# Kernel optimization log

Hardware: AMD Instinct MI355X
Metric: run time of the kernel (lower is better)

The kernel has to match this reference:

```python
import jax, jax.numpy as jnp
import numpy as np


def rotary_pos_emb(x):
    # x: [b, h, l, k]; interleaved rotary embedding (pairs are (0,1),(2,3),...)
    dim = x.shape[-1]
    seq = x.shape[-2]
    ts = jnp.arange(0, dim, 2, dtype=jnp.float32)
    inv_freqs = 10000.0 ** (-ts / dim)                      # [dim/2]
    grid = jnp.arange(seq, dtype=jnp.float32)[:, None] * inv_freqs[None, :]  # [l, dim/2]
    sin_embs = jnp.repeat(jnp.sin(grid), 2, axis=-1)[None]  # [1, l, dim] (interleaved repeat)
    cos_embs = jnp.repeat(jnp.cos(grid), 2, axis=-1)[None]
    x1, x2 = x[..., ::2], x[..., 1::2]
    xs = jnp.stack([-x2, x1], axis=-1).reshape(x.shape)     # interleave (-x2, x1)
    return x * cos_embs + xs * sin_embs


def setup_inputs() -> dict:
    key = jax.random.key(0)
    ks = jax.random.split(key, 5)
    b, l, d = 2, 2048, 1024
    scale = 1.0 / np.sqrt(d)
    return {
        "x": jax.random.normal(ks[0], (b, l, d), dtype=jnp.float32),
        "Wq": jax.random.normal(ks[1], (d, d), dtype=jnp.float32) * scale,
        "Wk": jax.random.normal(ks[2], (d, d), dtype=jnp.float32) * scale,
        "Wv": jax.random.normal(ks[3], (d, d), dtype=jnp.float32) * scale,
        "Wo": jax.random.normal(ks[4], (d, d), dtype=jnp.float32) * scale,
        "is_training": 0,
    }


def reference(x, Wq, Wk, Wv, Wo, is_training):
    n_heads = 16
    b, l, d = x.shape
    k_size = d // n_heads
    # NOTE: module scales q by 1/sqrt(model_size), not 1/sqrt(key_size)
    q = (x @ Wq) / jnp.sqrt(jnp.float32(d))
    q = q.reshape(b, l, n_heads, k_size).transpose(0, 2, 1, 3)  # b h l k
    k = (x @ Wk).reshape(b, l, n_heads, k_size).transpose(0, 2, 1, 3)
    v = (x @ Wv).reshape(b, l, n_heads, k_size).transpose(0, 2, 1, 3)
    q = rotary_pos_emb(q)
    k = rotary_pos_emb(k)
    logits = jnp.einsum('bhik,bhjk->bhij', q, k)  # no mask, no dropout (eval)
    a = jax.nn.softmax(logits, axis=-1)
    y = jnp.einsum('bhij,bhjv->bhiv', a, v)
    y = y.transpose(0, 2, 1, 3).reshape(b, l, d)  # b l (h v)
    return y @ Wo
```

## Files before the change

### kernel.cpp

```cpp
#include <hip/hip_runtime.h>
#include <stdint.h>

typedef unsigned short u16;
typedef unsigned int u32;
using short8 = __attribute__((ext_vector_type(8))) short;
using f32x4  = __attribute__((ext_vector_type(4))) float;
using f32x16 = __attribute__((ext_vector_type(16))) float;

typedef __attribute__((address_space(1))) unsigned int gu32;
typedef __attribute__((address_space(3))) unsigned int lu32;

__device__ __forceinline__ void gl2lds16(const u16* g, u16* lds_wave_base) {
    __builtin_amdgcn_global_load_lds(
        (gu32*)(uintptr_t)(const void*)g,
        (lu32*)(uint32_t)(uintptr_t)(void*)lds_wave_base,
        16, 0, 0);
}

__device__ inline float bf2f(u16 u) {
    union { unsigned int i; float f; } v;
    v.i = ((unsigned int)u) << 16;
    return v.f;
}
__device__ inline u16 f2bf(float f) {
    union { float f; unsigned int i; } v;
    v.f = f;
    unsigned int x = v.i;
    return (u16)((x + 0x7fffu + ((x >> 16) & 1u)) >> 16);
}
__device__ inline u32 f2bf_trunc_u32(float f) {
    union { float f; unsigned int i; } v;
    v.f = f;
    return v.i >> 16;
}

__global__ __launch_bounds__(256) void prep(
    const float* __restrict__ x, u16* __restrict__ xb,
    const float* __restrict__ w0, const float* __restrict__ w1,
    const float* __restrict__ w2, const float* __restrict__ w3,
    u16* __restrict__ t0, u16* __restrict__ t1,
    u16* __restrict__ t2, u16* __restrict__ t3,
    float2* __restrict__ tab)
{
    int tx = threadIdx.x, ty = threadIdx.y;
    int tid = ty * 32 + tx;
    int z = blockIdx.z;
    if (z == 4) {
        int bidx = blockIdx.y * 32 + blockIdx.x;
        if (bidx < 256) {
            int idx = bidx * 256 + tid;
            int pos = idx >> 5, pi = idx & 31;
            const float l2_10000_over_32 = 0.41524101186f;
            float ang = (float)pos *
                __builtin_amdgcn_exp2f(-(float)pi * l2_10000_over_32);
            float sn, cs;
            __sincosf(ang, &sn, &cs);
            tab[idx] = make_float2(cs, sn);
        }
        return;
    }
    if (z >= 5) {
        int i = (((z - 5) * 1024 + blockIdx.y * 32 + blockIdx.x) * 256 + tid) * 4;
        float4 v = *(const float4*)(x + i);
        ushort4 o;
        o.x = f2bf(v.x); o.y = f2bf(v.y); o.z = f2bf(v.z); o.w = f2bf(v.w);
        *(ushort4*)(xb + i) = o;
        return;
    }
    __shared__ u16 tile[32][33];
    const float* src; u16* dst;
    switch (z) {
        case 0:  src = w0; dst = t0; break;
        case 1:  src = w1; dst = t1; break;
        case 2:  src = w2; dst = t2; break;
        default: src = w3; dst = t3; break;
    }
    int c0 = blockIdx.x * 32, r0 = blockIdx.y * 32;
    #pragma unroll
    for (int i = 0; i < 4; i++)
        tile[ty + i * 8][tx] = f2bf(src[(size_t)(r0 + ty + i * 8) * 1024 + c0 + tx]);
    __syncthreads();
    #pragma unroll
    for (int i = 0; i < 4; i++)
        dst[(size_t)(c0 + ty + i * 8) * 1024 + r0 + tx] = tile[tx][ty + i * 8];
}

__global__ __launch_bounds__(256) void gemm_qkv(
    const u16* __restrict__ A, const u16* __restrict__ Bt,
    const float2* __restrict__ ropetab,
    u16* __restrict__ Qb, u16* __restrict__ Kb, u16* __restrict__ VT)
{
    __shared__ __align__(16) char smem[24576];
    u16* As = (u16*)smem;
    u16* Bs = (u16*)(smem + 16384);

    const int tid  = threadIdx.x;
    const int lane = tid & 63;
    const int wid  = tid >> 6;
    const int quad = lane >> 4;
    const int l15  = lane & 15;
    const int wm   = wid >> 1, wn = wid & 1;

    const int m0 = blockIdx.y * 128;
    const int n0 = blockIdx.x * 64;
    const int mat = n0 >> 10;
    const int ln0 = n0 & 1023;

    f32x4 acc[4][2] = {};

    for (int k0 = 0; k0 < 1024; k0 += 64) {
        #pragma unroll
        for (int it = 0; it < 4; it++) {
            int c   = it * 256 + tid;
            int row = c >> 3;
            int col = ((c & 7) ^ (row & 7)) * 8;
            gl2lds16(&A[(size_t)(m0 + row) * 1024 + k0 + col],
                     &As[(size_t)(it * 256 + wid * 64) * 8]);
        }
        #pragma unroll
        for (int it = 0; it < 2; it++) {
            int c   = it * 256 + tid;
            int row = c >> 3;
            int col = ((c & 7) ^ (row & 7)) * 8;
            gl2lds16(&Bt[(size_t)(n0 + row) * 1024 + k0 + col],
                     &Bs[(size_t)(it * 256 + wid * 64) * 8]);
        }
        __syncthreads();

        #pragma unroll
        for (int s = 0; s < 2; s++) {
            short8 a[4], b[2];
            #pragma unroll
            for (int i = 0; i < 4; i++) {
                int ra = wm * 64 + i * 16 + l15;
                a[i] = *(const short8*)(&As[ra * 64 + (((s * 4 + quad) ^ (ra & 7)) * 8)]);
            }
            #pragma unroll
            for (int j = 0; j < 2; j++) {
                int rb = wn * 32 + j * 16 + l15;
                b[j] = *(const short8*)(&Bs[rb * 64 + (((s * 4 + quad) ^ (rb & 7)) * 8)]);
            }
            #pragma unroll
            for (int i = 0; i < 4; i++)
                #pragma unroll
                for (int j = 0; j < 2; j++)
                    acc[i][j] = __builtin_amdgcn_mfma_f32_16x16x32_bf16(a[i], b[j], acc[i][j], 0, 0, 0);
        }
        __syncthreads();
    }

    if (mat < 2) {
        u16* C = (mat == 0) ? Qb : Kb;
        const float scale = (mat == 0) ? (0.03125f * 1.44269504f) : 1.0f;
        const int odd = l15 & 1;
        #pragma unroll
        for (int i = 0; i < 4; i++)
            #pragma unroll
            for (int j = 0; j < 2; j++)
                #pragma unroll
                for (int r = 0; r < 4; r++) {
                    int lrow = wm * 64 + i * 16 + quad * 4 + r;
                    int col  = ln0 + wn * 32 + j * 16 + l15;
                    int pos  = (m0 + lrow) & 2047;
                    float v  = acc[i][j][r] * scale;
                    float vp = __shfl_xor(v, 1);
                    float2 sc = ropetab[pos * 32 + ((col & 63) >> 1)];
                    float outv = odd ? (v * sc.x + vp * sc.y)
                                     : (v * sc.x - vp * sc.y);
                    C[(size_t)(m0 + lrow) * 1024 + col] = f2bf(outv);
                }
    } else {
        u16* T = (u16*)smem;
        __syncthreads();
        const int qp = ((quad & 1) << 1) | (quad >> 1);
        #pragma unroll
        for (int i = 0; i < 4; i++)
            #pragma unroll
            for (int j = 0; j < 2; j++)
                #pragma unroll
                for (int r = 0; r < 4; r++) {
                    int prow = wm * 64 + i * 16 + qp * 4 + r;
                    int lcol = wn * 32 + j * 16 + l15;
                    T[lcol * 136 + prow] = f2bf(acc[i][j][r]);
                }
        __syncthreads();
        int bb2 = m0 >> 11, pos0 = m0 & 2047, h2 = ln0 >> 6;
        #pragma unroll
        for (int itc = 0; itc < 4; itc++) {
            int c  = itc * 256 + tid;
            int ch = c >> 4;
            int px = (c & 15) * 8;
            size_t dst = ((size_t)(bb2 * 16 + h2) * 64 + ch) * 2048
                         + pos0 + px;
            *(uint4*)(&VT[dst]) = *(const uint4*)(&T[ch * 136 + px]);
        }
    }
}

__global__ __launch_bounds__(256) void gemm_out(
    const u16* __restrict__ A, const u16* __restrict__ Bt, float* __restrict__ C)
{
    __shared__ __align__(16) u16 As[128 * 64];
    __shared__ __align__(16) u16 Bs[64 * 64];

    const int tid  = threadIdx.x;
    const int lane = tid & 63;
    const int wid  = tid >> 6;
    const int quad = lane >> 4;
    const int l15  = lane & 15;
    const int wm   = wid >> 1, wn = wid & 1;

    const int m0 = blockIdx.y * 128;
    const int n0 = blockIdx.x * 64;

    f32x4 acc[4][2] = {};

    for (int k0 = 0; k0 < 1024; k0 += 64) {
        #pragma unroll
        for (int it = 0; it < 4; it++) {
            int c   = it * 256 + tid;
            int row = c >> 3;
            int col = ((c & 7) ^ (row & 7)) * 8;
            gl2lds16(&A[(size_t)(m0 + row) * 1024 + k0 + col],
                     &As[(size_t)(it * 256 + wid * 64) * 8]);
        }
        #pragma unroll
        for (int it = 0; it < 2; it++) {
            int c   = it * 256 + tid;
            int row = c >> 3;
            int col = ((c & 7) ^ (row & 7)) * 8;
            gl2lds16(&Bt[(size_t)(n0 + row) * 1024 + k0 + col],
                     &Bs[(size_t)(it * 256 + wid * 64) * 8]);
        }
        __syncthreads();

        #pragma unroll
        for (int s = 0; s < 2; s++) {
            short8 a[4], b[2];
            #pragma unroll
            for (int i = 0; i < 4; i++) {
                int ra = wm * 64 + i * 16 + l15;
                a[i] = *(const short8*)(&As[ra * 64 + (((s * 4 + quad) ^ (ra & 7)) * 8)]);
            }
            #pragma unroll
            for (int j = 0; j < 2; j++) {
                int rb = wn * 32 + j * 16 + l15;
                b[j] = *(const short8*)(&Bs[rb * 64 + (((s * 4 + quad) ^ (rb & 7)) * 8)]);
            }
            #pragma unroll
            for (int i = 0; i < 4; i++)
                #pragma unroll
                for (int j = 0; j < 2; j++)
                    acc[i][j] = __builtin_amdgcn_mfma_f32_16x16x32_bf16(a[i], b[j], acc[i][j], 0, 0, 0);
        }
        __syncthreads();
    }

    #pragma unroll
    for (int i = 0; i < 4; i++)
        #pragma unroll
        for (int j = 0; j < 2; j++)
            #pragma unroll
            for (int r = 0; r < 4; r++) {
                int row = m0 + wm * 64 + i * 16 + quad * 4 + r;
                int col = n0 + wn * 32 + j * 16 + l15;
                C[(size_t)row * 1024 + col] = acc[i][j][r];
            }
}

__global__ __launch_bounds__(256, 2) void attn(
    const u16* __restrict__ Q, const u16* __restrict__ Kb,
    const u16* __restrict__ VT, u16* __restrict__ Y)
{
    __shared__ __align__(16) u16 Ks [128 * 68];
    __shared__ __align__(16) u16 VTs[64 * 128];

    const int tid  = threadIdx.x;
    const int lane = tid & 63, wid = tid >> 6;
    const int l31  = lane & 31, hi = lane >> 5;

    const int bh = blockIdx.x;
    const int qt = blockIdx.y;
    const int bb = bh >> 4, h = bh & 15;

    const size_t base = ((size_t)bb * 2048) * 1024 + (size_t)h * 64;

    short8 qf[4];
    {
        const u16* qp = Q + base
                      + ((size_t)qt * 128 + wid * 32 + l31) * 1024 + hi * 8;
        #pragma unroll
        for (int s = 0; s < 4; s++)
            qf[s] = *(const short8*)(qp + s * 16);
    }

    const int c0 = tid,        c1 = 256 + tid,
              c2 = 512 + tid,  c3 = 768 + tid;
    const int rk0 = c0 >> 3, ck0 = ((c0 & 7) ^ (rk0 & 7)) * 8;
    const int rk1 = c1 >> 3, ck1 = ((c1 & 7) ^ (rk1 & 7)) * 8;
    const int rk2 = c2 >> 3, ck2 = ((c2 & 7) ^ (rk2 & 7)) * 8;
    const int rk3 = c3 >> 3, ck3 = ((c3 & 7) ^ (rk3 & 7)) * 8;
    const int rv0 = c0 >> 4, cv0 = ((c0 & 15) ^ (rv0 & 15)) * 8;
    const int rv1 = c1 >> 4, cv1 = ((c1 & 15) ^ (rv1 & 15)) * 8;
    const int rv2 = c2 >> 4, cv2 = ((c2 & 15) ^ (rv2 & 15)) * 8;
    const int rv3 = c3 >> 4, cv3 = ((c3 & 15) ^ (rv3 & 15)) * 8;
    const int dK0 = rk0 * 68 + (c0 & 7) * 8, dK1 = rk1 * 68 + (c1 & 7) * 8;
    const int dK2 = rk2 * 68 + (c2 & 7) * 8, dK3 = rk3 * 68 + (c3 & 7) * 8;
    const u16* pK = Kb + base;
    const u16* pV = VT + ((size_t)bh * 64) * 2048;
    const size_t oK0 = (size_t)rk0 * 1024 + ck0, oK1 = (size_t)rk1 * 1024 + ck1;
    const size_t oK2 = (size_t)rk2 * 1024 + ck2, oK3 = (size_t)rk3 * 1024 + ck3;
    const size_t oV0 = (size_t)rv0 * 2048 + cv0, oV1 = (size_t)rv1 * 2048 + cv1;
    const size_t oV2 = (size_t)rv2 * 2048 + cv2, oV3 = (size_t)rv3 * 2048 + cv3;

    uint4 k0r, k1r, k2r, k3r, v0r, v1r, v2r, v3r;
#define LOADREGS(J0)                                                        \
    do {                                                                    \
        const size_t jk = (size_t)(J0) * 1024;                              \
        k0r = *(const uint4*)(pK + jk + oK0);                               \
        k1r = *(const uint4*)(pK + jk + oK1);                               \
        k2r = *(const uint4*)(pK + jk + oK2);                               \
        k3r = *(const uint4*)(pK + jk + oK3);                               \
        v0r = *(const uint4*)(pV + (J0) + oV0);                             \
        v1r = *(const uint4*)(pV + (J0) + oV1);                             \
        v2r = *(const uint4*)(pV + (J0) + oV2);                             \
        v3r = *(const uint4*)(pV + (J0) + oV3);                             \
    } while (0)

    f32x16 o0 = {}, o1 = {};
    float lsum = 0.0f;

    LOADREGS(0);

    for (int j0 = 0; j0 < 2048; j0 += 128) {
        __syncthreads();
        *(uint4*)(&Ks [dK0]) = k0r;
        *(uint4*)(&Ks [dK1]) = k1r;
        *(uint4*)(&Ks [dK2]) = k2r;
        *(uint4*)(&Ks [dK3]) = k3r;
        *(uint4*)(&VTs[(0 * 256 + tid) * 8]) = v0r;
        *(uint4*)(&VTs[(1 * 256 + tid) * 8]) = v1r;
        *(uint4*)(&VTs[(2 * 256 + tid) * 8]) = v2r;
        *(uint4*)(&VTs[(3 * 256 + tid) * 8]) = v3r;
        if (j0 + 128 < 2048)
            LOADREGS(j0 + 128);
        __syncthreads();

        f32x16 st[4];
        #pragma unroll
        for (int t = 0; t < 4; t++) {
            int key = t * 32 + l31;
            f32x16 z = {};
            __builtin_amdgcn_s_setprio(1);
            #pragma unroll
            for (int s = 0; s < 4; s++) {
                int chunk = ((2 * s + hi) ^ (key & 7)) * 8;
                short8 kf = *(const short8*)(&Ks[key * 68 + chunk]);
                z = __builtin_amdgcn_mfma_f32_32x32x16_bf16(kf, qf[s], z, 0, 0, 0);
            }
            __builtin_amdgcn_s_setprio(0);
            st[t] = z;
        }

        u32 X[4][4], Y[4][4];
        #pragma unroll
        for (int t = 0; t < 4; t++)
            #pragma unroll
            for (int g = 0; g < 4; g++) {
                float p0 = __builtin_amdgcn_exp2f(st[t][4 * g + 0]);
                float p1 = __builtin_amdgcn_exp2f(st[t][4 * g + 1]);
                float p2 = __builtin_amdgcn_exp2f(st[t][4 * g + 2]);
                float p3 = __builtin_amdgcn_exp2f(st[t][4 * g + 3]);
                lsum += (p0 + p1) + (p2 + p3);
                X[t][g] = f2bf_trunc_u32(p0) | (f2bf_trunc_u32(p1) << 16);
                Y[t][g] = f2bf_trunc_u32(p2) | (f2bf_trunc_u32(p3) << 16);
            }

        #pragma unroll
        for (int c16 = 0; c16 < 8; ++c16) {
            const int t = c16 >> 1, u = c16 & 1;
            union { u32 u4[4]; short8 s8; } pk;
            pk.u4[0] = X[t][2 * u];
            pk.u4[1] = Y[t][2 * u];
            pk.u4[2] = X[t][2 * u + 1];
            pk.u4[3] = Y[t][2 * u + 1];
            const int kch = 2 * c16 + hi;
            short8 v0 = *(const short8*)(&VTs[l31 * 128 + ((kch ^ (l31 & 15)) * 8)]);
            short8 v1 = *(const short8*)(&VTs[(32 + l31) * 128 + ((kch ^ ((32 + l31) & 15)) * 8)]);
            __builtin_amdgcn_s_setprio(1);
            o0 = __builtin_amdgcn_mfma_f32_32x32x16_bf16(pk.s8, v0, o0, 0, 0, 0);
            o1 = __builtin_amdgcn_mfma_f32_32x32x16_bf16(pk.s8, v1, o1, 0, 0, 0);
            __builtin_amdgcn_s_setprio(0);
        }
    }
#undef LOADREGS

    lsum += __shfl_xor(lsum, 32);
    float linv = 1.0f / lsum;

    size_t qrow0 = (size_t)qt * 128 + wid * 32;
    #pragma unroll
    for (int half = 0; half < 2; half++) {
        f32x16 o = half ? o1 : o0;
        #pragma unroll
        for (int reg = 0; reg < 16; reg++) {
            int qrow = (reg & 3) + 8 * (reg >> 2) + 4 * hi;
            float nv = o[reg] * __shfl(linv, qrow);
            Y[base + (qrow0 + qrow) * 1024 + half * 32 + l31] = f2bf(nv);
        }
    }
}

extern "C" void kernel_launch(void* const* d_in, const int* in_sizes, int n_in,
                              void* d_out, int out_size, void* d_ws, size_t ws_size,
                              hipStream_t stream)
{
    const float* x  = (const float*)d_in[0];
    const float* Wq = (const float*)d_in[1];
    const float* Wk = (const float*)d_in[2];
    const float* Wv = (const float*)d_in[3];
    const float* Wo = (const float*)d_in[4];
    float* out = (float*)d_out;

    char* ws = (char*)d_ws;
    u16*    xb    = (u16*)   (ws + (0ull  << 20));
    u16*    WqkvT = (u16*)   (ws + (8ull  << 20));
    u16*    WoT   = (u16*)   (ws + (14ull << 20));
    u16*    Qb    = (u16*)   (ws + (16ull << 20));
    u16*    Kb    = (u16*)   (ws + (24ull << 20));
    u16*    VTb   = (u16*)   (ws + (32ull << 20));
    u16*    Yb    = (u16*)   (ws + (40ull << 20));
    float2* tab   = (float2*)(ws + (48ull << 20));

    prep<<<dim3(32, 32, 9), dim3(32, 8), 0, stream>>>(
        x, xb, Wq, Wk, Wv, Wo,
        WqkvT, WqkvT + (1024ull * 1024), WqkvT + (2048ull * 1024), WoT, tab);
    gemm_qkv<<<dim3(48, 32), 256, 0, stream>>>(xb, WqkvT, tab, Qb, Kb, VTb);
    attn<<<dim3(32, 16), 256, 0, stream>>>(Qb, Kb, VTb, Yb);
    gemm_out<<<dim3(16, 32), 256, 0, stream>>>(Yb, WoT, out);
}
```

Baseline: 182.5 us.

## Split attention key tiles across wave pairs and halve query tile per block

The attention block now covers 64 query rows instead of 128, and each pair of waves shares 32 query rows while splitting each 128-key tile between them. After the loop the partial outputs and row sums are exchanged through shared memory and combined. This doubles the grid to 1024 blocks, cuts per-wave register use (launch bound raised to 4 blocks per SIMD group), and is aimed at better occupancy and latency hiding. In exchange, each K/V tile is loaded by twice as many blocks, and the final reduction adds an extra shared-memory pass.

New measurement: 224.9 us. +23.2%, slower.

```diff
diff --git a/kernel.cpp b/kernel.cpp
--- a/kernel.cpp
+++ b/kernel.cpp
@@ -268,7 +268,7 @@
             }
 }
 
-__global__ __launch_bounds__(256, 2) void attn(
+__global__ __launch_bounds__(256, 4) void attn(
     const u16* __restrict__ Q, const u16* __restrict__ Kb,
     const u16* __restrict__ VT, u16* __restrict__ Y)
 {
@@ -278,6 +278,8 @@
     const int tid  = threadIdx.x;
     const int lane = tid & 63, wid = tid >> 6;
     const int l31  = lane & 31, hi = lane >> 5;
+    const int rg   = wid >> 1;
+    const int wk   = wid & 1;
 
     const int bh = blockIdx.x;
     const int qt = blockIdx.y;
@@ -288,7 +290,7 @@
     short8 qf[4];
     {
         const u16* qp = Q + base
-                      + ((size_t)qt * 128 + wid * 32 + l31) * 1024 + hi * 8;
+                      + ((size_t)qt * 64 + rg * 32 + l31) * 1024 + hi * 8;
         #pragma unroll
         for (int s = 0; s < 4; s++)
             qf[s] = *(const short8*)(qp + s * 16);
@@ -308,10 +310,10 @@
     const int dK2 = rk2 * 68 + (c2 & 7) * 8, dK3 = rk3 * 68 + (c3 & 7) * 8;
     const u16* pK = Kb + base;
     const u16* pV = VT + ((size_t)bh * 64) * 2048;
-    const size_t oK0 = (size_t)rk0 * 1024 + ck0, oK1 = (size_t)rk1 * 1024 + ck1;
-    const size_t oK2 = (size_t)rk2 * 1024 + ck2, oK3 = (size_t)rk3 * 1024 + ck3;
-    const size_t oV0 = (size_t)rv0 * 2048 + cv0, oV1 = (size_t)rv1 * 2048 + cv1;
-    const size_t oV2 = (size_t)rv2 * 2048 + cv2, oV3 = (size_t)rv3 * 2048 + cv3;
+    const u32 oK0 = (u32)(rk0 * 1024 + ck0), oK1 = (u32)(rk1 * 1024 + ck1);
+    const u32 oK2 = (u32)(rk2 * 1024 + ck2), oK3 = (u32)(rk3 * 1024 + ck3);
+    const u32 oV0 = (u32)(rv0 * 2048 + cv0), oV1 = (u32)(rv1 * 2048 + cv1);
+    const u32 oV2 = (u32)(rv2 * 2048 + cv2), oV3 = (u32)(rv3 * 2048 + cv3);
 
     uint4 k0r, k1r, k2r, k3r, v0r, v1r, v2r, v3r;
 #define LOADREGS(J0)                                                        \
@@ -346,10 +348,10 @@
             LOADREGS(j0 + 128);
         __syncthreads();
 
-        f32x16 st[4];
-        #pragma unroll
-        for (int t = 0; t < 4; t++) {
-            int key = t * 32 + l31;
+        u32 X[2][4], Yp[2][4];
+        #pragma unroll
+        for (int tl = 0; tl < 2; tl++) {
+            const int key = wk * 64 + tl * 32 + l31;
             f32x16 z = {};
             __builtin_amdgcn_s_setprio(1);
             #pragma unroll
@@ -359,31 +361,27 @@
                 z = __builtin_amdgcn_mfma_f32_32x32x16_bf16(kf, qf[s], z, 0, 0, 0);
             }
             __builtin_amdgcn_s_setprio(0);
-            st[t] = z;
-        }
-
-        u32 X[4][4], Y[4][4];
-        #pragma unroll
-        for (int t = 0; t < 4; t++)
             #pragma unroll
             for (int g = 0; g < 4; g++) {
-                float p0 = __builtin_amdgcn_exp2f(st[t][4 * g + 0]);
-                float p1 = __builtin_amdgcn_exp2f(st[t][4 * g + 1]);
-                float p2 = __builtin_amdgcn_exp2f(st[t][4 * g + 2]);
-                float p3 = __builtin_amdgcn_exp2f(st[t][4 * g + 3]);
+                float p0 = __builtin_amdgcn_exp2f(z[4 * g + 0]);
+                float p1 = __builtin_amdgcn_exp2f(z[4 * g + 1]);
+                float p2 = __builtin_amdgcn_exp2f(z[4 * g + 2]);
+                float p3 = __builtin_amdgcn_exp2f(z[4 * g + 3]);
                 lsum += (p0 + p1) + (p2 + p3);
-                X[t][g] = f2bf_trunc_u32(p0) | (f2bf_trunc_u32(p1) << 16);
-                Y[t][g] = f2bf_trunc_u32(p2) | (f2bf_trunc_u32(p3) << 16);
-            }
-
-        #pragma unroll
-        for (int c16 = 0; c16 < 8; ++c16) {
-            const int t = c16 >> 1, u = c16 & 1;
+                X [tl][g] = f2bf_trunc_u32(p0) | (f2bf_trunc_u32(p1) << 16);
+                Yp[tl][g] = f2bf_trunc_u32(p2) | (f2bf_trunc_u32(p3) << 16);
+            }
+        }
+
+        #pragma unroll
+        for (int d = 0; d < 4; ++d) {
+            const int tl = d >> 1, u = d & 1;
+            const int c16 = wk * 4 + d;
             union { u32 u4[4]; short8 s8; } pk;
-            pk.u4[0] = X[t][2 * u];
-            pk.u4[1] = Y[t][2 * u];
-            pk.u4[2] = X[t][2 * u + 1];
-            pk.u4[3] = Y[t][2 * u + 1];
+            pk.u4[0] = X [tl][2 * u];
+            pk.u4[1] = Yp[tl][2 * u];
+            pk.u4[2] = X [tl][2 * u + 1];
+            pk.u4[3] = Yp[tl][2 * u + 1];
             const int kch = 2 * c16 + hi;
             short8 v0 = *(const short8*)(&VTs[l31 * 128 + ((kch ^ (l31 & 15)) * 8)]);
             short8 v1 = *(const short8*)(&VTs[(32 + l31) * 128 + ((kch ^ ((32 + l31) & 15)) * 8)]);
@@ -396,18 +394,35 @@
 #undef LOADREGS
 
     lsum += __shfl_xor(lsum, 32);
-    float linv = 1.0f / lsum;
-
-    size_t qrow0 = (size_t)qt * 128 + wid * 32;
+
+    __syncthreads();
+    float* xo = (float*)Ks;
+    float* lb = (float*)VTs;
+    {
+        f32x16 give = wk ? o0 : o1;
+        float* wb = xo + wid * 1024;
+        #pragma unroll
+        for (int r = 0; r < 16; r++)
+            wb[r * 64 + lane] = give[r];
+        if (hi == 0) lb[wid * 32 + l31] = lsum;
+    }
+    __syncthreads();
+    const int pw = wid ^ 1;
+    f32x16 keep = wk ? o1 : o0;
+    {
+        const float* rb = xo + pw * 1024;
+        #pragma unroll
+        for (int r = 0; r < 16; r++)
+            keep[r] += rb[r * 64 + lane];
+    }
+    float linv = 1.0f / (lsum + lb[pw * 32 + l31]);
+
+    const size_t qrow0 = (size_t)qt * 64 + rg * 32;
     #pragma unroll
-    for (int half = 0; half < 2; half++) {
-        f32x16 o = half ? o1 : o0;
-        #pragma unroll
-        for (int reg = 0; reg < 16; reg++) {
-            int qrow = (reg & 3) + 8 * (reg >> 2) + 4 * hi;
-            float nv = o[reg] * __shfl(linv, qrow);
-            Y[base + (qrow0 + qrow) * 1024 + half * 32 + l31] = f2bf(nv);
-        }
+    for (int reg = 0; reg < 16; reg++) {
+        int qrow = (reg & 3) + 8 * (reg >> 2) + 4 * hi;
+        float nv = keep[reg] * __shfl(linv, qrow);
+        Y[base + (qrow0 + qrow) * 1024 + wk * 32 + l31] = f2bf(nv);
     }
 }
 
@@ -436,6 +451,6 @@
         x, xb, Wq, Wk, Wv, Wo,
         WqkvT, WqkvT + (1024ull * 1024), WqkvT + (2048ull * 1024), WoT, tab);
     gemm_qkv<<<dim3(48, 32), 256, 0, stream>>>(xb, WqkvT, tab, Qb, Kb, VTb);
-    attn<<<dim3(32, 16), 256, 0, stream>>>(Qb, Kb, VTb, Yb);
+    attn<<<dim3(32, 32), 256, 0, stream>>>(Qb, Kb, VTb, Yb);
     gemm_out<<<dim3(16, 32), 256, 0, stream>>>(Yb, WoT, out);
 }
```
